# Optimization experiments

Measured on AMD Instinct MI355X. Metric: run time of the kernel, lower is better.

## Reference

```python
import jax, jax.numpy as jnp
import numpy as np

B, N, D, C = 32, 4096, 512, 64
EPS = 1e-12  # F.normalize eps


def setup_inputs() -> dict:
    key = jax.random.key(0)
    k1, k2, k3 = jax.random.split(key, 3)
    x = jax.random.normal(k1, (B, N, D), dtype=jnp.float32)
    mask = jax.random.randint(k2, (B,), 1, N + 1, dtype=jnp.int64)  # num valid per batch, >=1
    anchors = jax.random.uniform(k3, (C, D), dtype=jnp.float32)  # torch.rand init
    return {"x": x, "mask": mask, "anchors": anchors}


def reference(x, mask, anchors):
    b, n, d = x.shape
    c = anchors.shape[0]
    # L2 normalize features along D (F.normalize, p=2, dim=2)
    xn = x / jnp.maximum(jnp.linalg.norm(x, axis=2, keepdims=True), EPS)
    # pairwise L2 distance to anchors via expansion (avoid [B,N,C,D] materialization)
    sq = (jnp.sum(xn * xn, axis=2, keepdims=True)            # [B,N,1]
          + jnp.sum(anchors * anchors, axis=1)[None, None, :]  # [1,1,C]
          - 2.0 * jnp.einsum('bnd,cd->bnc', xn, anchors))      # [B,N,C]
    dist = jnp.sqrt(jnp.maximum(sq, 0.0))  # [B,N,C]
    valid = jnp.arange(n)[None, :] < mask[:, None]  # [B,N] bool
    # masked softmax over clusters of inverse distance; invalid rows -> 0
    score = jax.nn.softmax(1.0 / dist, axis=2)
    score = jnp.where(valid[:, :, None], score, 0.0)  # [B,N,C]
    # hard assignment and per-batch mode cluster (bincount+argmax, vectorized)
    attribute = jnp.argmax(score, axis=2)  # [B,N]
    counts = jnp.sum(jax.nn.one_hot(attribute, c, dtype=score.dtype)
                     * valid[:, :, None].astype(score.dtype), axis=1)  # [B,C]
    index = jnp.argmax(counts, axis=1)  # [B] mode cluster id
    # weights[i] = score[i, :, index[i]]
    weights = jnp.take_along_axis(score, index[:, None, None], axis=2)[..., 0]  # [B,N]
    feature = jnp.sum(xn * weights[:, :, None], axis=1)  # [B,D]
    return feature
```

## Files before the change

### kernel.cpp

```cpp
#include <hip/hip_runtime.h>

constexpr int BB = 32;
constexpr int NN = 4096;
constexpr int DD = 512;
constexpr int CC = 64;

constexpr int BM = 64;
constexpr int BK = 16;
constexpr int MROWS = BB * NN;
constexpr int NBLK1 = MROWS / BM;

constexpr size_t WS_SCORES = 0;
constexpr size_t WS_INVN   = (size_t)BB * CC * NN;
constexpr size_t WS_COUNTS = WS_INVN + (size_t)BB * NN;
constexpr size_t WS_INDEX  = WS_COUNTS + (size_t)BB * CC;
constexpr size_t WS_ANORM  = WS_INDEX + BB;

__global__ __launch_bounds__(256) void k0_init(const float* __restrict__ anchors,
                                               float* __restrict__ out,
                                               int* __restrict__ counts,
                                               float* __restrict__ anorm2)
{
    int t = blockIdx.x * 256 + threadIdx.x;
    if (t < BB * DD) out[t] = 0.0f;
    if (t < BB * CC) counts[t] = 0;
    if (blockIdx.x == 0 && threadIdx.x < CC) {
        const float4* a = (const float4*)(anchors + (size_t)threadIdx.x * DD);
        float s = 0.f;
        for (int i = 0; i < DD / 4; ++i) {
            float4 v = a[i];
            s += v.x * v.x + v.y * v.y + v.z * v.z + v.w * v.w;
        }
        anorm2[threadIdx.x] = s;
    }
}

__global__ __launch_bounds__(256) void k1_scores(
    const float* __restrict__ x, const int* __restrict__ mask,
    const float* __restrict__ anchors, const float* __restrict__ anorm2,
    float* __restrict__ scoresT, float* __restrict__ invn,
    int* __restrict__ counts)
{
    __shared__ float xt[BK][BM + 4];
    __shared__ float at[BK][CC + 4];
    __shared__ float dl[BM][CC + 4];
    __shared__ float rssq[BM];
    __shared__ float an2[CC];

    const int t = threadIdx.x;
    const int brow = blockIdx.x * BM;
    const int srow = t >> 2;
    const int kq   = t & 3;
    const int tc   = t >> 4;
    const int tm   = t & 15;

    if (t < CC) an2[t] = anorm2[t];

    const float* xp = x + (size_t)(brow + srow) * DD + kq * 4;
    const float* ap = anchors + (size_t)srow * DD + kq * 4;

    float acc[4][4] = {};
    float ssq = 0.f;

    float4 xv = *(const float4*)(xp);
    float4 av = *(const float4*)(ap);

    for (int kb = 0; kb < DD; kb += BK) {
        ssq += xv.x * xv.x + xv.y * xv.y + xv.z * xv.z + xv.w * xv.w;
        xt[kq * 4 + 0][srow] = xv.x; xt[kq * 4 + 1][srow] = xv.y;
        xt[kq * 4 + 2][srow] = xv.z; xt[kq * 4 + 3][srow] = xv.w;
        at[kq * 4 + 0][srow] = av.x; at[kq * 4 + 1][srow] = av.y;
        at[kq * 4 + 2][srow] = av.z; at[kq * 4 + 3][srow] = av.w;
        __syncthreads();
        if (kb + BK < DD) {
            xv = *(const float4*)(xp + kb + BK);
            av = *(const float4*)(ap + kb + BK);
        }
        #pragma unroll
        for (int k = 0; k < BK; ++k) {
            float4 xf = *(const float4*)&xt[k][tm * 4];
            float4 af = *(const float4*)&at[k][tc * 4];
            float xr[4] = {xf.x, xf.y, xf.z, xf.w};
            float ar[4] = {af.x, af.y, af.z, af.w};
            #pragma unroll
            for (int i = 0; i < 4; ++i)
                #pragma unroll
                for (int j = 0; j < 4; ++j)
                    acc[i][j] += xr[i] * ar[j];
        }
        __syncthreads();
    }

    ssq += __shfl_xor(ssq, 1);
    ssq += __shfl_xor(ssq, 2);
    if (kq == 0) rssq[srow] = ssq;

    #pragma unroll
    for (int i = 0; i < 4; ++i) {
        float4 v4 = make_float4(acc[i][0], acc[i][1], acc[i][2], acc[i][3]);
        *(float4*)&dl[tm * 4 + i][tc * 4] = v4;
    }
    __syncthreads();

    const int r = srow;
    const int q = kq;
    const int gn = brow + r;
    const int b  = gn >> 12;
    const int n  = gn & (NN - 1);
    const float ss = rssq[r];
    float nrm = fmaxf(sqrtf(ss), 1e-12f);
    const float inv  = 1.0f / nrm;
    const float ssqn = ss * inv * inv;

    float v[16];
    float vmax = -3.4e38f;
    #pragma unroll
    for (int j = 0; j < 16; ++j) {
        const int c = q * 16 + j;
        float dot = dl[r][c] * inv;
        float sq = fmaxf(ssqn + an2[c] - 2.0f * dot, 0.0f);
        float dist = sqrtf(sq);
        float vv = 1.0f / dist;
        v[j] = vv;
        vmax = fmaxf(vmax, vv);
    }
    float bv = v[0]; int bc = q * 16;
    #pragma unroll
    for (int j = 1; j < 16; ++j)
        if (v[j] > bv) { bv = v[j]; bc = q * 16 + j; }

    vmax = fmaxf(vmax, __shfl_xor(vmax, 1));
    vmax = fmaxf(vmax, __shfl_xor(vmax, 2));
    float s = 0.f;
    #pragma unroll
    for (int j = 0; j < 16; ++j) { float e = __expf(v[j] - vmax); v[j] = e; s += e; }
    s += __shfl_xor(s, 1);
    s += __shfl_xor(s, 2);
    const float rs = 1.0f / s;

    #pragma unroll
    for (int d = 1; d <= 2; d <<= 1) {
        float ov = __shfl_xor(bv, d);
        int   oc = __shfl_xor(bc, d);
        if (ov > bv || (ov == bv && oc < bc)) { bv = ov; bc = oc; }
    }

    const bool valid = (n < mask[b]);
    const float vm = valid ? 1.0f : 0.0f;
    float* so = scoresT + ((size_t)b * CC) * NN + n;
    #pragma unroll
    for (int j = 0; j < 16; ++j)
        so[(size_t)(q * 16 + j) * NN] = v[j] * rs * vm;

    if (q == 0) {
        invn[gn] = inv;
        if (valid) atomicAdd(&counts[b * CC + bc], 1);
    }
}

__global__ void k2_index(const int* __restrict__ counts, int* __restrict__ index)
{
    const int c = threadIdx.x;
    for (int b = 0; b < BB; ++b) {
        int cnt = counts[b * CC + c];
        int bc = c;
        #pragma unroll
        for (int d = 1; d < 64; d <<= 1) {
            int ocnt = __shfl_xor(cnt, d);
            int oc   = __shfl_xor(bc, d);
            if (ocnt > cnt || (ocnt == cnt && oc < bc)) { cnt = ocnt; bc = oc; }
        }
        if (c == 0) index[b] = bc;
    }
}

constexpr int NCHUNK = 16;
constexpr int CROWS = NN / NCHUNK;
__global__ __launch_bounds__(256) void k3_feature(
    const float* __restrict__ x, const float* __restrict__ scoresT,
    const float* __restrict__ invn, const int* __restrict__ index,
    float* __restrict__ out)
{
    __shared__ float w[CROWS];
    const int t  = threadIdx.x;
    const int b  = blockIdx.x >> 4;
    const int ch = blockIdx.x & (NCHUNK - 1);
    const int n0 = ch * CROWS;
    const int idx = index[b];
    {
        const int n = n0 + t;
        float sc = scoresT[((size_t)(b * CC + idx)) * NN + n];
        w[t] = sc * invn[(size_t)b * NN + n];
    }
    __syncthreads();

    float ax = 0.f, ay = 0.f;
    const float* xb = x + ((size_t)b * NN + n0) * DD + t * 2;
    for (int r0 = 0; r0 < CROWS; r0 += 8) {
        #pragma unroll
        for (int u = 0; u < 8; ++u) {
            float2 xv = *(const float2*)(xb + (size_t)(r0 + u) * DD);
            float ww = w[r0 + u];
            ax += xv.x * ww;
            ay += xv.y * ww;
        }
    }
    atomicAdd(&out[b * DD + t * 2],     ax);
    atomicAdd(&out[b * DD + t * 2 + 1], ay);
}

extern "C" void kernel_launch(void* const* d_in, const int* in_sizes, int n_in,
                              void* d_out, int out_size, void* d_ws, size_t ws_size,
                              hipStream_t stream)
{
    const float* x       = (const float*)d_in[0];
    const int*   mask    = (const int*)d_in[1];
    const float* anchors = (const float*)d_in[2];
    float* out = (float*)d_out;

    float* wsf     = (float*)d_ws;
    float* scoresT = wsf + WS_SCORES;
    float* invn    = wsf + WS_INVN;
    int*   counts  = (int*)(wsf + WS_COUNTS);
    int*   index   = (int*)(wsf + WS_INDEX);
    float* anorm2  = wsf + WS_ANORM;

    hipLaunchKernelGGL(k0_init,  dim3(64),           dim3(256), 0, stream,
                       anchors, out, counts, anorm2);
    hipLaunchKernelGGL(k1_scores, dim3(NBLK1),       dim3(256), 0, stream,
                       x, mask, anchors, anorm2, scoresT, invn, counts);
    hipLaunchKernelGGL(k2_index, dim3(1),            dim3(64),  0, stream,
                       counts, index);
    hipLaunchKernelGGL(k3_feature, dim3(BB * NCHUNK), dim3(256), 0, stream,
                       x, scoresT, invn, index, out);
}
```

Measured before the change: 564.6 us.

## Enlarge GEMM tile, compute softmax in registers, store scores row-major

The score kernel now uses 128-row by 32-deep tiles with an 8x4 register microtile per thread. The softmax, argmax and count logic runs directly on the accumulators with 16-lane shuffles, which removes the shared-memory staging of the dot products. Scores are written row-major as float4 stores instead of strided transposed stores. The feature kernel is reorganised into many more, smaller blocks with float4 loads, so the weight gather now reads a strided column and more atomics hit the output.

```diff
diff --git a/kernel.cpp b/kernel.cpp
--- a/kernel.cpp
+++ b/kernel.cpp
@@ -5,13 +5,13 @@
 constexpr int DD = 512;
 constexpr int CC = 64;
 
-constexpr int BM = 64;
-constexpr int BK = 16;
+constexpr int BM = 128;
+constexpr int BK = 32;
 constexpr int MROWS = BB * NN;
 constexpr int NBLK1 = MROWS / BM;
 
 constexpr size_t WS_SCORES = 0;
-constexpr size_t WS_INVN   = (size_t)BB * CC * NN;
+constexpr size_t WS_INVN   = (size_t)BB * NN * CC;
 constexpr size_t WS_COUNTS = WS_INVN + (size_t)BB * NN;
 constexpr size_t WS_INDEX  = WS_COUNTS + (size_t)BB * CC;
 constexpr size_t WS_ANORM  = WS_INDEX + BB;
@@ -27,6 +27,7 @@
     if (blockIdx.x == 0 && threadIdx.x < CC) {
         const float4* a = (const float4*)(anchors + (size_t)threadIdx.x * DD);
         float s = 0.f;
+        #pragma unroll 8
         for (int i = 0; i < DD / 4; ++i) {
             float4 v = a[i];
             s += v.x * v.x + v.y * v.y + v.z * v.z + v.w * v.w;
@@ -38,123 +39,136 @@
 __global__ __launch_bounds__(256) void k1_scores(
     const float* __restrict__ x, const int* __restrict__ mask,
     const float* __restrict__ anchors, const float* __restrict__ anorm2,
-    float* __restrict__ scoresT, float* __restrict__ invn,
+    float* __restrict__ scores, float* __restrict__ invn,
     int* __restrict__ counts)
 {
     __shared__ float xt[BK][BM + 4];
     __shared__ float at[BK][CC + 4];
-    __shared__ float dl[BM][CC + 4];
     __shared__ float rssq[BM];
-    __shared__ float an2[CC];
-
-    const int t = threadIdx.x;
+    __shared__ float an2s[CC];
+
+    const int t    = threadIdx.x;
     const int brow = blockIdx.x * BM;
-    const int srow = t >> 2;
-    const int kq   = t & 3;
-    const int tc   = t >> 4;
-    const int tm   = t & 15;
-
-    if (t < CC) an2[t] = anorm2[t];
-
-    const float* xp = x + (size_t)(brow + srow) * DD + kq * 4;
-    const float* ap = anchors + (size_t)srow * DD + kq * 4;
-
-    float acc[4][4] = {};
+    const int b    = brow >> 12;
+    const int n0   = brow & (NN - 1);
+    const int tc   = t & 15;
+    const int tm   = t >> 4;
+
+    const int sxrow = t >> 1;
+    const int sxk   = (t & 1) * 16;
+    const int sac   = t & 63;
+    const int sak   = (t >> 6) * 8;
+
+    if (t < CC) an2s[t] = anorm2[t];
+
+    const float* xp = x + (size_t)(brow + sxrow) * DD + sxk;
+    const float* ap = anchors + (size_t)sac * DD + sak;
+
+    float4 xr0 = *(const float4*)(xp + 0);
+    float4 xr1 = *(const float4*)(xp + 4);
+    float4 xr2 = *(const float4*)(xp + 8);
+    float4 xr3 = *(const float4*)(xp + 12);
+    float4 ar0 = *(const float4*)(ap + 0);
+    float4 ar1 = *(const float4*)(ap + 4);
+
+    float acc[8][4] = {};
     float ssq = 0.f;
 
-    float4 xv = *(const float4*)(xp);
-    float4 av = *(const float4*)(ap);
-
     for (int kb = 0; kb < DD; kb += BK) {
-        ssq += xv.x * xv.x + xv.y * xv.y + xv.z * xv.z + xv.w * xv.w;
-        xt[kq * 4 + 0][srow] = xv.x; xt[kq * 4 + 1][srow] = xv.y;
-        xt[kq * 4 + 2][srow] = xv.z; xt[kq * 4 + 3][srow] = xv.w;
-        at[kq * 4 + 0][srow] = av.x; at[kq * 4 + 1][srow] = av.y;
-        at[kq * 4 + 2][srow] = av.z; at[kq * 4 + 3][srow] = av.w;
+        ssq += xr0.x*xr0.x + xr0.y*xr0.y + xr0.z*xr0.z + xr0.w*xr0.w
+             + xr1.x*xr1.x + xr1.y*xr1.y + xr1.z*xr1.z + xr1.w*xr1.w
+             + xr2.x*xr2.x + xr2.y*xr2.y + xr2.z*xr2.z + xr2.w*xr2.w
+             + xr3.x*xr3.x + xr3.y*xr3.y + xr3.z*xr3.z + xr3.w*xr3.w;
+        xt[sxk +  0][sxrow] = xr0.x; xt[sxk +  1][sxrow] = xr0.y;
+        xt[sxk +  2][sxrow] = xr0.z; xt[sxk +  3][sxrow] = xr0.w;
+        xt[sxk +  4][sxrow] = xr1.x; xt[sxk +  5][sxrow] = xr1.y;
+        xt[sxk +  6][sxrow] = xr1.z; xt[sxk +  7][sxrow] = xr1.w;
+        xt[sxk +  8][sxrow] = xr2.x; xt[sxk +  9][sxrow] = xr2.y;
+        xt[sxk + 10][sxrow] = xr2.z; xt[sxk + 11][sxrow] = xr2.w;
+        xt[sxk + 12][sxrow] = xr3.x; xt[sxk + 13][sxrow] = xr3.y;
+        xt[sxk + 14][sxrow] = xr3.z; xt[sxk + 15][sxrow] = xr3.w;
+        at[sak + 0][sac] = ar0.x; at[sak + 1][sac] = ar0.y;
+        at[sak + 2][sac] = ar0.z; at[sak + 3][sac] = ar0.w;
+        at[sak + 4][sac] = ar1.x; at[sak + 5][sac] = ar1.y;
+        at[sak + 6][sac] = ar1.z; at[sak + 7][sac] = ar1.w;
         __syncthreads();
         if (kb + BK < DD) {
-            xv = *(const float4*)(xp + kb + BK);
-            av = *(const float4*)(ap + kb + BK);
+            xr0 = *(const float4*)(xp + kb + BK + 0);
+            xr1 = *(const float4*)(xp + kb + BK + 4);
+            xr2 = *(const float4*)(xp + kb + BK + 8);
+            xr3 = *(const float4*)(xp + kb + BK + 12);
+            ar0 = *(const float4*)(ap + kb + BK + 0);
+            ar1 = *(const float4*)(ap + kb + BK + 4);
         }
         #pragma unroll
         for (int k = 0; k < BK; ++k) {
-            float4 xf = *(const float4*)&xt[k][tm * 4];
-            float4 af = *(const float4*)&at[k][tc * 4];
-            float xr[4] = {xf.x, xf.y, xf.z, xf.w};
-            float ar[4] = {af.x, af.y, af.z, af.w};
+            float4 x0 = *(const float4*)&xt[k][tm * 8];
+            float4 x1 = *(const float4*)&xt[k][tm * 8 + 4];
+            float4 a0 = *(const float4*)&at[k][tc * 4];
+            float xv[8] = {x0.x, x0.y, x0.z, x0.w, x1.x, x1.y, x1.z, x1.w};
+            float av[4] = {a0.x, a0.y, a0.z, a0.w};
             #pragma unroll
-            for (int i = 0; i < 4; ++i)
+            for (int i = 0; i < 8; ++i)
                 #pragma unroll
                 for (int j = 0; j < 4; ++j)
-                    acc[i][j] += xr[i] * ar[j];
+                    acc[i][j] += xv[i] * av[j];
         }
         __syncthreads();
     }
 
     ssq += __shfl_xor(ssq, 1);
-    ssq += __shfl_xor(ssq, 2);
-    if (kq == 0) rssq[srow] = ssq;
+    if ((t & 1) == 0) rssq[sxrow] = ssq;
+    __syncthreads();
+
+    const int mval = mask[b];
 
     #pragma unroll
-    for (int i = 0; i < 4; ++i) {
-        float4 v4 = make_float4(acc[i][0], acc[i][1], acc[i][2], acc[i][3]);
-        *(float4*)&dl[tm * 4 + i][tc * 4] = v4;
-    }
-    __syncthreads();
-
-    const int r = srow;
-    const int q = kq;
-    const int gn = brow + r;
-    const int b  = gn >> 12;
-    const int n  = gn & (NN - 1);
-    const float ss = rssq[r];
-    float nrm = fmaxf(sqrtf(ss), 1e-12f);
-    const float inv  = 1.0f / nrm;
-    const float ssqn = ss * inv * inv;
-
-    float v[16];
-    float vmax = -3.4e38f;
-    #pragma unroll
-    for (int j = 0; j < 16; ++j) {
-        const int c = q * 16 + j;
-        float dot = dl[r][c] * inv;
-        float sq = fmaxf(ssqn + an2[c] - 2.0f * dot, 0.0f);
-        float dist = sqrtf(sq);
-        float vv = 1.0f / dist;
-        v[j] = vv;
-        vmax = fmaxf(vmax, vv);
-    }
-    float bv = v[0]; int bc = q * 16;
-    #pragma unroll
-    for (int j = 1; j < 16; ++j)
-        if (v[j] > bv) { bv = v[j]; bc = q * 16 + j; }
-
-    vmax = fmaxf(vmax, __shfl_xor(vmax, 1));
-    vmax = fmaxf(vmax, __shfl_xor(vmax, 2));
-    float s = 0.f;
-    #pragma unroll
-    for (int j = 0; j < 16; ++j) { float e = __expf(v[j] - vmax); v[j] = e; s += e; }
-    s += __shfl_xor(s, 1);
-    s += __shfl_xor(s, 2);
-    const float rs = 1.0f / s;
-
-    #pragma unroll
-    for (int d = 1; d <= 2; d <<= 1) {
-        float ov = __shfl_xor(bv, d);
-        int   oc = __shfl_xor(bc, d);
-        if (ov > bv || (ov == bv && oc < bc)) { bv = ov; bc = oc; }
-    }
-
-    const bool valid = (n < mask[b]);
-    const float vm = valid ? 1.0f : 0.0f;
-    float* so = scoresT + ((size_t)b * CC) * NN + n;
-    #pragma unroll
-    for (int j = 0; j < 16; ++j)
-        so[(size_t)(q * 16 + j) * NN] = v[j] * rs * vm;
-
-    if (q == 0) {
-        invn[gn] = inv;
-        if (valid) atomicAdd(&counts[b * CC + bc], 1);
+    for (int i = 0; i < 8; ++i) {
+        const int R = tm * 8 + i;
+        const int n = n0 + R;
+        const float ss   = rssq[R];
+        const float inv  = 1.0f / fmaxf(sqrtf(ss), 1e-12f);
+        const float ssqn = ss * inv * inv;
+
+        float v[4];
+        #pragma unroll
+        for (int j = 0; j < 4; ++j) {
+            const int c = tc * 4 + j;
+            float sq = fmaxf(ssqn + an2s[c] - 2.0f * (acc[i][j] * inv), 0.0f);
+            v[j] = 1.0f / sqrtf(sq);
+        }
+        float vmax = fmaxf(fmaxf(v[0], v[1]), fmaxf(v[2], v[3]));
+        #pragma unroll
+        for (int d = 1; d <= 8; d <<= 1) vmax = fmaxf(vmax, __shfl_xor(vmax, d));
+
+        float e[4]; float s = 0.f;
+        #pragma unroll
+        for (int j = 0; j < 4; ++j) { e[j] = __expf(v[j] - vmax); s += e[j]; }
+        #pragma unroll
+        for (int d = 1; d <= 8; d <<= 1) s += __shfl_xor(s, d);
+        const float rs = 1.0f / s;
+
+        float bv = v[0]; int bc = tc * 4;
+        #pragma unroll
+        for (int j = 1; j < 4; ++j)
+            if (v[j] > bv) { bv = v[j]; bc = tc * 4 + j; }
+        #pragma unroll
+        for (int d = 1; d <= 8; d <<= 1) {
+            float ov = __shfl_xor(bv, d);
+            int   oc = __shfl_xor(bc, d);
+            if (ov > bv || (ov == bv && oc < bc)) { bv = ov; bc = oc; }
+        }
+
+        const bool valid = (n < mval);
+        const float vm = valid ? 1.0f : 0.0f;
+        float4 sv = make_float4(e[0] * rs * vm, e[1] * rs * vm,
+                                e[2] * rs * vm, e[3] * rs * vm);
+        *(float4*)&scores[((size_t)(b * NN + n)) * CC + tc * 4] = sv;
+
+        if (tc == 0) {
+            invn[(size_t)b * NN + n] = inv;
+            if (valid) atomicAdd(&counts[b * CC + bc], 1);
+        }
     }
 }
 
@@ -174,39 +188,39 @@
     }
 }
 
-constexpr int NCHUNK = 16;
-constexpr int CROWS = NN / NCHUNK;
+constexpr int K3_ROWS = 64;
+constexpr int K3_BLOCKS = MROWS / K3_ROWS;
 __global__ __launch_bounds__(256) void k3_feature(
-    const float* __restrict__ x, const float* __restrict__ scoresT,
+    const float* __restrict__ x, const float* __restrict__ scores,
     const float* __restrict__ invn, const int* __restrict__ index,
     float* __restrict__ out)
 {
-    __shared__ float w[CROWS];
-    const int t  = threadIdx.x;
-    const int b  = blockIdx.x >> 4;
-    const int ch = blockIdx.x & (NCHUNK - 1);
-    const int n0 = ch * CROWS;
+    __shared__ float w[K3_ROWS];
+    const int t   = threadIdx.x;
+    const int blk = blockIdx.x;
+    const int b   = blk >> 6;
+    const int n0  = (blk & 63) * K3_ROWS;
     const int idx = index[b];
-    {
+    if (t < K3_ROWS) {
         const int n = n0 + t;
-        float sc = scoresT[((size_t)(b * CC + idx)) * NN + n];
-        w[t] = sc * invn[(size_t)b * NN + n];
+        w[t] = scores[((size_t)(b * NN + n)) * CC + idx] * invn[(size_t)b * NN + n];
     }
     __syncthreads();
 
-    float ax = 0.f, ay = 0.f;
-    const float* xb = x + ((size_t)b * NN + n0) * DD + t * 2;
-    for (int r0 = 0; r0 < CROWS; r0 += 8) {
-        #pragma unroll
-        for (int u = 0; u < 8; ++u) {
-            float2 xv = *(const float2*)(xb + (size_t)(r0 + u) * DD);
-            float ww = w[r0 + u];
-            ax += xv.x * ww;
-            ay += xv.y * ww;
-        }
-    }
-    atomicAdd(&out[b * DD + t * 2],     ax);
-    atomicAdd(&out[b * DD + t * 2 + 1], ay);
+    const int d0 = (t & 127) * 4;
+    const int rh = (t >> 7) * 32;
+    const float* xb = x + ((size_t)b * NN + n0 + rh) * DD + d0;
+    float a0 = 0.f, a1 = 0.f, a2 = 0.f, a3 = 0.f;
+    #pragma unroll 8
+    for (int r = 0; r < 32; ++r) {
+        float4 xv = *(const float4*)(xb + (size_t)r * DD);
+        float ww = w[rh + r];
+        a0 += xv.x * ww; a1 += xv.y * ww; a2 += xv.z * ww; a3 += xv.w * ww;
+    }
+    atomicAdd(&out[b * DD + d0 + 0], a0);
+    atomicAdd(&out[b * DD + d0 + 1], a1);
+    atomicAdd(&out[b * DD + d0 + 2], a2);
+    atomicAdd(&out[b * DD + d0 + 3], a3);
 }
 
 extern "C" void kernel_launch(void* const* d_in, const int* in_sizes, int n_in,
@@ -219,18 +233,18 @@
     float* out = (float*)d_out;
 
     float* wsf     = (float*)d_ws;
-    float* scoresT = wsf + WS_SCORES;
+    float* scores  = wsf + WS_SCORES;
     float* invn    = wsf + WS_INVN;
     int*   counts  = (int*)(wsf + WS_COUNTS);
     int*   index   = (int*)(wsf + WS_INDEX);
     float* anorm2  = wsf + WS_ANORM;
 
-    hipLaunchKernelGGL(k0_init,  dim3(64),           dim3(256), 0, stream,
+    hipLaunchKernelGGL(k0_init,   dim3(64),        dim3(256), 0, stream,
                        anchors, out, counts, anorm2);
-    hipLaunchKernelGGL(k1_scores, dim3(NBLK1),       dim3(256), 0, stream,
-                       x, mask, anchors, anorm2, scoresT, invn, counts);
-    hipLaunchKernelGGL(k2_index, dim3(1),            dim3(64),  0, stream,
+    hipLaunchKernelGGL(k1_scores, dim3(NBLK1),     dim3(256), 0, stream,
+                       x, mask, anchors, anorm2, scores, invn, counts);
+    hipLaunchKernelGGL(k2_index,  dim3(1),         dim3(64),  0, stream,
                        counts, index);
-    hipLaunchKernelGGL(k3_feature, dim3(BB * NCHUNK), dim3(256), 0, stream,
-                       x, scoresT, invn, index, out);
-}
+    hipLaunchKernelGGL(k3_feature, dim3(K3_BLOCKS), dim3(256), 0, stream,
+                       x, scores, invn, index, out);
+}
```

New measurement: 553.9 us. About the same (-1.9%).
